# Optimization experiments

Measured on AMD Instinct MI355X. Metric: run time of the kernel, lower is better.

## Reference

```python
import jax, jax.numpy as jnp
import numpy as np

HEADS = 8
D_K = 64
LN_EPS = 1e-6


def setup_inputs() -> dict:
    key = jax.random.key(0)
    ks = jax.random.split(key, 12)
    B, S, D = 4, 2048, 512
    inp = {
        "key": jax.random.normal(ks[0], (B, S, D), jnp.float32),
        "value": jax.random.normal(ks[1], (B, S, D), jnp.float32),
        "query": jax.random.normal(ks[2], (B, S, D), jnp.float32),
        "mask": jax.random.randint(ks[3], (B, S, S), 0, 2).astype(bool),
        # projection weights (torch Linear: y = x @ W.T + b)
        "Wk": jax.random.normal(ks[4], (D, D), jnp.float32) * (1.0 / np.sqrt(D)),
        "bk": jnp.zeros((D,), jnp.float32),
        "Wv": jax.random.normal(ks[5], (D, D), jnp.float32) * (1.0 / np.sqrt(D)),
        "bv": jnp.zeros((D,), jnp.float32),
        "Wq": jax.random.normal(ks[6], (D, D), jnp.float32) * (1.0 / np.sqrt(D)),
        "bq": jnp.zeros((D,), jnp.float32),
        # LayerNorm gain/bias
        "a2": jnp.ones((D,), jnp.float32),
        "b2": jnp.zeros((D,), jnp.float32),
    }
    return inp


def _attention(key, value, query, mask, Wk, bk, Wv, bv, Wq, bq, a2, b2):
    B, Sq, D = query.shape
    Sk = key.shape[1]
    H, dk = HEADS, D_K

    def split_heads(x, W, b):
        y = x @ W.T + b                                   # [B, S, D]
        return y.reshape(x.shape[0], x.shape[1], H, dk).transpose(0, 2, 1, 3)  # [B,H,S,dk]

    k_up = split_heads(key, Wk, bk)
    v_up = split_heads(value, Wv, bv)
    q_up = split_heads(query, Wq, bq)

    # scaled dot-product scores, full [B,H,Sq,Sk] matrix (as in the original bmm)
    scores = jnp.einsum("bhqd,bhkd->bhqk", q_up, k_up) / jnp.sqrt(jnp.asarray(dk, scores_dtype(q_up)))
    scores = jnp.where(mask[:, None, :, :], -jnp.inf, scores)
    attn = jax.nn.softmax(scores, axis=-1)                # dropout p=0 -> identity

    out = jnp.einsum("bhqk,bhkd->bhqd", attn, v_up)       # [B,H,Sq,dk]
    out = out.transpose(0, 2, 1, 3).reshape(B, Sq, D)
    res = out + query                                     # residual (res_dropout p=0)

    # OpenNMT LayerNorm: (x - mu) / (std + eps) * a2 + b2, unbiased std
    mu = res.mean(axis=-1, keepdims=True)
    var = jnp.sum((res - mu) ** 2, axis=-1, keepdims=True) / (D - 1)
    res = a2 * (res - mu) / (jnp.sqrt(var) + LN_EPS) + b2

    attn_flat = attn.reshape(B * H, Sq, Sk)               # matches torch [B*H, Sq, Sk]
    return res, attn_flat


def scores_dtype(x):
    return x.dtype


def reference(key, value, query, mask, Wk, bk, Wv, bv, Wq, bq, a2, b2):
    return _attention(key, value, query, mask, Wk, bk, Wv, bv, Wq, bq, a2, b2)
```

## Files before the change

### kernel.cpp

```cpp
#include <hip/hip_runtime.h>
#include <stdint.h>

typedef float f32x4 __attribute__((ext_vector_type(4)));
typedef short bf16x8 __attribute__((ext_vector_type(8)));

constexpr int NB = 4;
constexpr int NS = 2048;
constexpr int ND = 512;
constexpr int NH = 8;
constexpr int NDK = 64;
constexpr int NT = NS / 64;
constexpr float QSCALE = 0.125f * 1.44269504088896340736f;

static __device__ __forceinline__ unsigned short f2bf(float f) {
    union { float f; uint32_t u; } v; v.f = f;
    uint32_t r = (v.u + 0x7FFFu + ((v.u >> 16) & 1u)) >> 16;
    return (unsigned short)r;
}
static __device__ __forceinline__ unsigned short f2bf_fast(float f) {
    union { float f; uint32_t u; } v; v.f = f;
    return (unsigned short)((v.u + 0x8000u) >> 16);
}
static __device__ __forceinline__ float exp2_fast(float x) {
#if __has_builtin(__builtin_amdgcn_exp2f)
    return __builtin_amdgcn_exp2f(x);
#else
    return exp2f(x);
#endif
}

static __device__ __forceinline__ void gload_lds16(const void* g, void* l) {
    __builtin_amdgcn_global_load_lds((const __attribute__((address_space(1))) void*)g,
                                     (__attribute__((address_space(3))) void*)l, 16, 0, 0);
}

__global__ __launch_bounds__(256) void cvt3_kernel(const float4* __restrict__ a,
                                                   const float4* __restrict__ b,
                                                   const float4* __restrict__ c,
                                                   ushort4* __restrict__ oa,
                                                   ushort4* __restrict__ ob,
                                                   ushort4* __restrict__ oc, int n4) {
    int which = blockIdx.y;
    const float4* in = which == 0 ? a : which == 1 ? b : c;
    ushort4* out = which == 0 ? oa : which == 1 ? ob : oc;
    int i = blockIdx.x * blockDim.x + threadIdx.x;
    if (i >= n4) return;
    float4 v = in[i];
    ushort4 o;
    o.x = f2bf(v.x); o.y = f2bf(v.y); o.z = f2bf(v.z); o.w = f2bf(v.w);
    out[i] = o;
}

__global__ __launch_bounds__(256) void bitmask_kernel(const int* __restrict__ mask,
                                                      unsigned long long* __restrict__ bm,
                                                      int nwords) {
    int lane = threadIdx.x & 63;
    int wave = threadIdx.x >> 6;
    int wgid = blockIdx.x * 4 + wave;
    int nw = gridDim.x * 4;
    for (int c = wgid; c < nwords; c += nw) {
        int v = mask[(size_t)c * 64 + lane];
        unsigned long long bits = __ballot(v != 0);
        if (lane == 0) bm[c] = bits;
    }
}

__global__ __launch_bounds__(256) void proj_kernel(const unsigned short* __restrict__ xq,
                                                   const unsigned short* __restrict__ xk,
                                                   const unsigned short* __restrict__ xv,
                                                   const unsigned short* __restrict__ wq,
                                                   const unsigned short* __restrict__ wk,
                                                   const unsigned short* __restrict__ wv,
                                                   const float* __restrict__ bq,
                                                   const float* __restrict__ bk,
                                                   const float* __restrict__ bv,
                                                   unsigned short* __restrict__ Qw,
                                                   unsigned short* __restrict__ Kw,
                                                   unsigned short* __restrict__ VTw) {
    int z = blockIdx.z;
    const unsigned short* X = z == 0 ? xq : z == 1 ? xk : xv;
    const unsigned short* W = z == 0 ? wq : z == 1 ? wk : wv;
    const float* bias = z == 0 ? bq : z == 1 ? bk : bv;
    unsigned short* out = z == 0 ? Qw : z == 1 ? Kw : VTw;
    float scale = z == 0 ? QSCALE : 1.0f;
    int vtrans = (z == 2);

    int lane = threadIdx.x & 63;
    int wave = threadIdx.x >> 6;
    int lrow = lane & 15, lgrp = lane >> 4;
    int m0 = blockIdx.x * 64 + wave * 16;
    int n0 = blockIdx.y * 64;

    f32x4 acc[4] = {{0.f,0.f,0.f,0.f},{0.f,0.f,0.f,0.f},{0.f,0.f,0.f,0.f},{0.f,0.f,0.f,0.f}};
    const unsigned short* xrow = X + (size_t)(m0 + lrow) * ND;
    for (int k = 0; k < ND; k += 32) {
        bf16x8 a = *(const bf16x8*)(xrow + k + lgrp * 8);
#pragma unroll
        for (int n = 0; n < 4; n++) {
            bf16x8 b = *(const bf16x8*)(W + (size_t)(n0 + n * 16 + lrow) * ND + k + lgrp * 8);
            acc[n] = __builtin_amdgcn_mfma_f32_16x16x32_bf16(a, b, acc[n], 0, 0, 0);
        }
    }
#pragma unroll
    for (int n = 0; n < 4; n++) {
        int col = n0 + n * 16 + lrow;
        int h = col >> 6, d = col & 63;
        float bv_ = bias[col];
#pragma unroll
        for (int j = 0; j < 4; j++) {
            int m = m0 + lgrp * 4 + j;
            int bidx = m >> 11, s = m & (NS - 1);
            float y = (acc[n][j] + bv_) * scale;
            size_t off = vtrans ? ((size_t)(bidx * NH + h) * NDK + d) * NS + s
                                : ((size_t)(bidx * NH + h) * NS + s) * NDK + d;
            out[off] = f2bf(y);
        }
    }
}

__global__ __launch_bounds__(512) void attn_kernel(const unsigned short* __restrict__ Q,
                                                   const unsigned short* __restrict__ K,
                                                   const unsigned short* __restrict__ VT,
                                                   const unsigned long long* __restrict__ bm,
                                                   float* __restrict__ attn_out,
                                                   float* __restrict__ Ob) {
    __shared__ __align__(16) unsigned short kb[2][64 * 64];
    __shared__ __align__(16) unsigned short vb[2][64 * 64];
    __shared__ __align__(16) unsigned short pl[8][16][80];

    int lane = threadIdx.x & 63;
    int wave = threadIdx.x >> 6;
    int lrow = lane & 15, lgrp = lane >> 4;

    int id = blockIdx.x;
    int xcd = id & 7;
    int loc = id >> 3;
    int bh = xcd * 4 + (loc >> 4);
    int qb = loc & 15;
    int b = bh >> 3, h = bh & 7;
    int qw = qb * 128 + wave * 16;

    const unsigned short* qrow = Q + ((size_t)bh * NS + qw + lrow) * NDK + lgrp * 8;
    bf16x8 aq0 = *(const bf16x8*)(qrow);
    bf16x8 aq1 = *(const bf16x8*)(qrow + 32);

    const unsigned short* kbase = K + (size_t)bh * NS * NDK;
    const unsigned short* vbase = VT + (size_t)bh * NDK * NS;
    const unsigned long long* bmb = bm + (size_t)b * NS * (NS / 64);
    int bmoff[4];
#pragma unroll
    for (int j = 0; j < 4; j++) bmoff[j] = (qw + lgrp * 4 + j) * (NS / 64);

    int rl = lane >> 3, cc = lane & 7;
    int cs = (cc ^ rl) * 8;

    {
        const unsigned short* s0 = kbase + (size_t)(8 * wave + rl) * NDK + cs;
        gload_lds16(s0, &kb[0][wave * 512]);
    }
    unsigned long long wc[4], wn[4];
#pragma unroll
    for (int j = 0; j < 4; j++) wc[j] = bmb[bmoff[j]];
    __syncthreads();

    float lacc[4] = {0.f, 0.f, 0.f, 0.f};
    for (int t = 0; t < NT; t++) {
        int buf = t & 1;
        int tn = (t + 1 < NT) ? t + 1 : t;
        if (t + 1 < NT) {
            const unsigned short* s0 = kbase + (size_t)(tn * 64 + 8 * wave + rl) * NDK + cs;
            gload_lds16(s0, &kb[buf ^ 1][wave * 512]);
        }
#pragma unroll
        for (int j = 0; j < 4; j++) wn[j] = bmb[bmoff[j] + tn];

        f32x4 sc[4] = {{0.f,0.f,0.f,0.f},{0.f,0.f,0.f,0.f},{0.f,0.f,0.f,0.f},{0.f,0.f,0.f,0.f}};
        __builtin_amdgcn_s_setprio(1);
#pragma unroll
        for (int n = 0; n < 4; n++) {
            int R = n * 16 + lrow;
            bf16x8 b0 = *(const bf16x8*)&kb[buf][R * 64 + ((lgrp ^ (lrow & 7)) * 8)];
            bf16x8 b1 = *(const bf16x8*)&kb[buf][R * 64 + (((4 + lgrp) ^ (lrow & 7)) * 8)];
            sc[n] = __builtin_amdgcn_mfma_f32_16x16x32_bf16(aq0, b0, sc[n], 0, 0, 0);
            sc[n] = __builtin_amdgcn_mfma_f32_16x16x32_bf16(aq1, b1, sc[n], 0, 0, 0);
        }
        __builtin_amdgcn_s_setprio(0);
#pragma unroll
        for (int j = 0; j < 4; j++) {
            uint32_t wlo = (uint32_t)wc[j], whi = (uint32_t)(wc[j] >> 32);
#pragma unroll
            for (int n = 0; n < 4; n++) {
                uint32_t bit = ((n < 2 ? wlo : whi) >> ((n & 1) * 16 + lrow)) & 1u;
                float e = exp2_fast(sc[n][j]);
                lacc[j] += bit ? 0.f : e;
            }
        }
#pragma unroll
        for (int j = 0; j < 4; j++) wc[j] = wn[j];
        __syncthreads();
    }
    float li[4];
#pragma unroll
    for (int j = 0; j < 4; j++) {
        float l = lacc[j];
        l += __shfl_xor(l, 1);
        l += __shfl_xor(l, 2);
        l += __shfl_xor(l, 4);
        l += __shfl_xor(l, 8);
        li[j] = -__log2f(l);
    }

    {
        const unsigned short* s0 = kbase + (size_t)(8 * wave + rl) * NDK + cs;
        gload_lds16(s0, &kb[0][wave * 512]);
        const unsigned short* s1 = vbase + (size_t)(8 * wave + rl) * NS + cs;
        gload_lds16(s1, &vb[0][wave * 512]);
    }
#pragma unroll
    for (int j = 0; j < 4; j++) wc[j] = bmb[bmoff[j]];
    __syncthreads();

    f32x4 accO[4] = {{0.f,0.f,0.f,0.f},{0.f,0.f,0.f,0.f},{0.f,0.f,0.f,0.f},{0.f,0.f,0.f,0.f}};
    float* aout = attn_out + (size_t)bh * NS * NS;
    float* abase[4];
#pragma unroll
    for (int j = 0; j < 4; j++) abase[j] = aout + (size_t)(qw + lgrp * 4 + j) * NS + lrow;

    float pst[4][4];
    for (int t = 0; t < NT; t++) {
        int buf = t & 1;
        int tn = (t + 1 < NT) ? t + 1 : t;
        if (t > 0) {
            int ktp = (t - 1) * 64;
#pragma unroll
            for (int n = 0; n < 4; n++)
#pragma unroll
                for (int j = 0; j < 4; j++)
                    abase[j][ktp + n * 16] = pst[n][j];
        }
        if (t + 1 < NT) {
            const unsigned short* s0 = kbase + (size_t)(tn * 64 + 8 * wave + rl) * NDK + cs;
            gload_lds16(s0, &kb[buf ^ 1][wave * 512]);
            const unsigned short* s1 = vbase + (size_t)(8 * wave + rl) * NS + tn * 64 + cs;
            gload_lds16(s1, &vb[buf ^ 1][wave * 512]);
        }
#pragma unroll
        for (int j = 0; j < 4; j++) wn[j] = bmb[bmoff[j] + tn];

        f32x4 sc[4] = {{0.f,0.f,0.f,0.f},{0.f,0.f,0.f,0.f},{0.f,0.f,0.f,0.f},{0.f,0.f,0.f,0.f}};
        __builtin_amdgcn_s_setprio(1);
#pragma unroll
        for (int n = 0; n < 4; n++) {
            int R = n * 16 + lrow;
            bf16x8 b0 = *(const bf16x8*)&kb[buf][R * 64 + ((lgrp ^ (lrow & 7)) * 8)];
            bf16x8 b1 = *(const bf16x8*)&kb[buf][R * 64 + (((4 + lgrp) ^ (lrow & 7)) * 8)];
            sc[n] = __builtin_amdgcn_mfma_f32_16x16x32_bf16(aq0, b0, sc[n], 0, 0, 0);
            sc[n] = __builtin_amdgcn_mfma_f32_16x16x32_bf16(aq1, b1, sc[n], 0, 0, 0);
        }
        __builtin_amdgcn_s_setprio(0);
#pragma unroll
        for (int j = 0; j < 4; j++) {
            uint32_t wlo = (uint32_t)wc[j], whi = (uint32_t)(wc[j] >> 32);
#pragma unroll
            for (int n = 0; n < 4; n++) {
                uint32_t bit = ((n < 2 ? wlo : whi) >> ((n & 1) * 16 + lrow)) & 1u;
                float p = bit ? 0.f : exp2_fast(sc[n][j] + li[j]);
                pst[n][j] = p;
                pl[wave][lgrp * 4 + j][n * 16 + lrow] = f2bf_fast(p);
            }
        }
        __builtin_amdgcn_s_setprio(1);
#pragma unroll
        for (int step = 0; step < 2; step++) {
            bf16x8 ap = *(const bf16x8*)&pl[wave][lrow][step * 32 + lgrp * 8];
#pragma unroll
            for (int n = 0; n < 4; n++) {
                int R = n * 16 + lrow;
                bf16x8 bv = *(const bf16x8*)&vb[buf][R * 64 + (((4 * step + lgrp) ^ (lrow & 7)) * 8)];
                accO[n] = __builtin_amdgcn_mfma_f32_16x16x32_bf16(ap, bv, accO[n], 0, 0, 0);
            }
        }
        __builtin_amdgcn_s_setprio(0);
#pragma unroll
        for (int j = 0; j < 4; j++) wc[j] = wn[j];
        __syncthreads();
    }
    {
        int ktp = (NT - 1) * 64;
#pragma unroll
        for (int n = 0; n < 4; n++)
#pragma unroll
            for (int j = 0; j < 4; j++)
                abase[j][ktp + n * 16] = pst[n][j];
    }

#pragma unroll
    for (int n = 0; n < 4; n++)
#pragma unroll
        for (int j = 0; j < 4; j++) {
            int qi = qw + lgrp * 4 + j;
            Ob[((size_t)b * NS + qi) * ND + h * NDK + n * 16 + lrow] = accO[n][j];
        }
}

__global__ __launch_bounds__(256) void ln_kernel(const float* __restrict__ Ob,
                                                 const float* __restrict__ query,
                                                 const float* __restrict__ a2,
                                                 const float* __restrict__ b2,
                                                 float* __restrict__ out) {
    int row = blockIdx.x * 4 + (threadIdx.x >> 6);
    int lane = threadIdx.x & 63;
    const float4* orow = (const float4*)(Ob + (size_t)row * ND);
    const float4* qrow = (const float4*)(query + (size_t)row * ND);
    float4 v[2];
    float sum = 0.f;
#pragma unroll
    for (int t = 0; t < 2; t++) {
        float4 o = orow[lane + t * 64];
        float4 q = qrow[lane + t * 64];
        v[t].x = o.x + q.x; v[t].y = o.y + q.y; v[t].z = o.z + q.z; v[t].w = o.w + q.w;
        sum += v[t].x + v[t].y + v[t].z + v[t].w;
    }
#pragma unroll
    for (int s = 1; s < 64; s <<= 1) sum += __shfl_xor(sum, s);
    float mu = sum * (1.f / ND);
    float sq = 0.f;
#pragma unroll
    for (int t = 0; t < 2; t++) {
        float dx = v[t].x - mu, dy = v[t].y - mu, dz = v[t].z - mu, dw = v[t].w - mu;
        sq += dx * dx + dy * dy + dz * dz + dw * dw;
    }
#pragma unroll
    for (int s = 1; s < 64; s <<= 1) sq += __shfl_xor(sq, s);
    float var = sq * (1.f / (ND - 1));
    float inv = 1.f / (sqrtf(var) + 1e-6f);
    float4* orow_out = (float4*)(out + (size_t)row * ND);
#pragma unroll
    for (int t = 0; t < 2; t++) {
        float4 g = ((const float4*)a2)[lane + t * 64];
        float4 bb = ((const float4*)b2)[lane + t * 64];
        float4 r;
        r.x = g.x * (v[t].x - mu) * inv + bb.x;
        r.y = g.y * (v[t].y - mu) * inv + bb.y;
        r.z = g.z * (v[t].z - mu) * inv + bb.z;
        r.w = g.w * (v[t].w - mu) * inv + bb.w;
        orow_out[lane + t * 64] = r;
    }
}

extern "C" void kernel_launch(void* const* d_in, const int* in_sizes, int n_in,
                              void* d_out, int out_size, void* d_ws, size_t ws_size,
                              hipStream_t stream) {
    const float* key   = (const float*)d_in[0];
    const float* value = (const float*)d_in[1];
    const float* query = (const float*)d_in[2];
    const int*   mask  = (const int*)d_in[3];
    const float* Wk = (const float*)d_in[4];
    const float* bk = (const float*)d_in[5];
    const float* Wv = (const float*)d_in[6];
    const float* bv = (const float*)d_in[7];
    const float* Wq = (const float*)d_in[8];
    const float* bq = (const float*)d_in[9];
    const float* a2 = (const float*)d_in[10];
    const float* b2 = (const float*)d_in[11];

    const size_t nX = (size_t)NB * NS * ND;
    const size_t nW = (size_t)ND * ND;
    const int    nBMw = NB * NS * NS / 64;

    unsigned short* xq  = (unsigned short*)d_ws;
    unsigned short* xk  = xq + nX;
    unsigned short* xv  = xk + nX;
    unsigned short* wqb = xv + nX;
    unsigned short* wkb = wqb + nW;
    unsigned short* wvb = wkb + nW;
    unsigned short* Qw  = wvb + nW;
    unsigned short* Kw  = Qw + nX;
    unsigned short* VTw = Kw + nX;
    float* Ow = (float*)(VTw + nX);
    unsigned long long* bmw = (unsigned long long*)(Ow + nX);

    bitmask_kernel<<<2048, 256, 0, stream>>>(mask, bmw, nBMw);

    cvt3_kernel<<<dim3((int)(nX / 4 / 256), 3), 256, 0, stream>>>(
        (const float4*)query, (const float4*)key, (const float4*)value,
        (ushort4*)xq, (ushort4*)xk, (ushort4*)xv, (int)(nX / 4));
    cvt3_kernel<<<dim3((int)(nW / 4 / 256), 3), 256, 0, stream>>>(
        (const float4*)Wq, (const float4*)Wk, (const float4*)Wv,
        (ushort4*)wqb, (ushort4*)wkb, (ushort4*)wvb, (int)(nW / 4));

    proj_kernel<<<dim3(128, 8, 3), 256, 0, stream>>>(xq, xk, xv, wqb, wkb, wvb,
                                                     bq, bk, bv, Qw, Kw, VTw);

    float* attn_out = (float*)d_out + nX;
    attn_kernel<<<512, 512, 0, stream>>>(Qw, Kw, VTw, bmw, attn_out, Ow);

    ln_kernel<<<2048, 256, 0, stream>>>(Ow, query, a2, b2, (float*)d_out);
}
```

Measured before the change: 397.9 us.

## Replace syncthreads with partial vmcnt waits so attn stores stay in flight

Swaps __syncthreads for explicit s_waitcnt plus s_barrier and skips the barrier after the last tile. In the second pass, attention probabilities are now stored directly in the tile where they are computed, and the barrier waits only until 16 or fewer memory ops are outstanding, so the 16 global stores need not drain before the next tile starts. The aim is to hide store latency behind the loads and MFMA work of the next tile. The vmcnt(16) count depends on how the compiler orders loads and stores, so correctness of the LDS prefetch wait is fragile.

```diff
diff --git a/kernel.cpp b/kernel.cpp
--- a/kernel.cpp
+++ b/kernel.cpp
@@ -161,7 +161,8 @@
     unsigned long long wc[4], wn[4];
 #pragma unroll
     for (int j = 0; j < 4; j++) wc[j] = bmb[bmoff[j]];
-    __syncthreads();
+    asm volatile("s_waitcnt vmcnt(0)" ::: "memory");
+    __builtin_amdgcn_s_barrier();
 
     float lacc[4] = {0.f, 0.f, 0.f, 0.f};
     for (int t = 0; t < NT; t++) {
@@ -197,7 +198,10 @@
         }
 #pragma unroll
         for (int j = 0; j < 4; j++) wc[j] = wn[j];
-        __syncthreads();
+        if (t + 1 < NT) {
+            asm volatile("s_waitcnt vmcnt(0)" ::: "memory");
+            __builtin_amdgcn_s_barrier();
+        }
     }
     float li[4];
 #pragma unroll
@@ -218,7 +222,8 @@
     }
 #pragma unroll
     for (int j = 0; j < 4; j++) wc[j] = bmb[bmoff[j]];
-    __syncthreads();
+    asm volatile("s_waitcnt vmcnt(0)" ::: "memory");
+    __builtin_amdgcn_s_barrier();
 
     f32x4 accO[4] = {{0.f,0.f,0.f,0.f},{0.f,0.f,0.f,0.f},{0.f,0.f,0.f,0.f},{0.f,0.f,0.f,0.f}};
     float* aout = attn_out + (size_t)bh * NS * NS;
@@ -226,18 +231,10 @@
 #pragma unroll
     for (int j = 0; j < 4; j++) abase[j] = aout + (size_t)(qw + lgrp * 4 + j) * NS + lrow;
 
-    float pst[4][4];
     for (int t = 0; t < NT; t++) {
         int buf = t & 1;
+        int kt = t * 64;
         int tn = (t + 1 < NT) ? t + 1 : t;
-        if (t > 0) {
-            int ktp = (t - 1) * 64;
-#pragma unroll
-            for (int n = 0; n < 4; n++)
-#pragma unroll
-                for (int j = 0; j < 4; j++)
-                    abase[j][ktp + n * 16] = pst[n][j];
-        }
         if (t + 1 < NT) {
             const unsigned short* s0 = kbase + (size_t)(tn * 64 + 8 * wave + rl) * NDK + cs;
             gload_lds16(s0, &kb[buf ^ 1][wave * 512]);
@@ -265,7 +262,7 @@
             for (int n = 0; n < 4; n++) {
                 uint32_t bit = ((n < 2 ? wlo : whi) >> ((n & 1) * 16 + lrow)) & 1u;
                 float p = bit ? 0.f : exp2_fast(sc[n][j] + li[j]);
-                pst[n][j] = p;
+                abase[j][kt + n * 16] = p;
                 pl[wave][lgrp * 4 + j][n * 16 + lrow] = f2bf_fast(p);
             }
         }
@@ -283,15 +280,10 @@
         __builtin_amdgcn_s_setprio(0);
 #pragma unroll
         for (int j = 0; j < 4; j++) wc[j] = wn[j];
-        __syncthreads();
-    }
-    {
-        int ktp = (NT - 1) * 64;
-#pragma unroll
-        for (int n = 0; n < 4; n++)
-#pragma unroll
-            for (int j = 0; j < 4; j++)
-                abase[j][ktp + n * 16] = pst[n][j];
+        if (t + 1 < NT) {
+            asm volatile("s_waitcnt vmcnt(16)" ::: "memory");
+            __builtin_amdgcn_s_barrier();
+        }
     }
 
 #pragma unroll
```

Result: faster. 360.1 us (-9.5%).
